# Kernel tuning notes

Hardware: AMD Instinct MI355X
Metric: run time of the kernel (lower is better)

## Reference

```python
import jax, jax.numpy as jnp
import numpy as np

NUM_HEADS = 16
HEAD_DIM = 80  # embed_dim 1280 / 16


def setup_inputs() -> dict:
    key = jax.random.key(0)
    ks = jax.random.split(key, 5)
    E = NUM_HEADS * HEAD_DIM
    sq, b = 1024, 8
    x = jax.random.normal(ks[0], (sq, b, E), dtype=jnp.float32)
    w_in = jax.random.normal(ks[1], (E, 3 * E), dtype=jnp.float32) * (E ** -0.5)
    b_in = jax.random.normal(ks[2], (3 * E,), dtype=jnp.float32) * 0.01
    w_out = jax.random.normal(ks[3], (E, E), dtype=jnp.float32) * (E ** -0.5)
    b_out = jax.random.normal(ks[4], (E,), dtype=jnp.float32) * 0.01
    return {"x": x, "w_in": w_in, "b_in": b_in, "w_out": w_out, "b_out": b_out}


def reference(x, w_in, b_in, w_out, b_out):
    sq, b, E = x.shape
    H, D = NUM_HEADS, HEAD_DIM
    norm_factor = jnp.asarray(D ** 0.5, x.dtype)
    # in_proj: [sq, b, 3E] -> [sq, b, H, 3D], split into q/k/v along last dim
    mixed = (x @ w_in + b_in).reshape(sq, b, H, 3 * D)
    q, k, v = jnp.split(mixed, 3, axis=-1)  # each [sq, b, H, D]
    # merge (b, H) and move to batch-of-bmm layout [b*H, sq, D]
    q = q.reshape(sq, b * H, D).transpose(1, 0, 2) / norm_factor
    k = k.reshape(sq, b * H, D).transpose(1, 0, 2)
    v = v.reshape(sq, b * H, D).transpose(1, 0, 2)
    scores = jnp.einsum('nqd,nkd->nqk', q, k)  # [b*H, sq, sq]
    probs = jax.nn.softmax(scores, axis=-1)
    ctx = jnp.einsum('nqk,nkd->nqd', probs, v)  # [b*H, sq, D]
    # [b, H, sq, D] -> [sq, b, H, D] -> [sq, b, E]
    ctx = ctx.reshape(b, H, sq, D).transpose(2, 0, 1, 3).reshape(sq, b, E)
    return ctx @ w_out + b_out
```

## Files before the change

### kernel.cpp

```cpp
#include <hip/hip_runtime.h>

#define DEVI __device__ __forceinline__

typedef _Float16 f16x8 __attribute__((ext_vector_type(8)));
typedef _Float16 f16x4v __attribute__((ext_vector_type(4)));
typedef _Float16 f16x2 __attribute__((ext_vector_type(2)));
typedef float f32x4 __attribute__((ext_vector_type(4)));

DEVI void gl16(const void* g, void* l) {
  __builtin_amdgcn_global_load_lds((const __attribute__((address_space(1))) void*)g,
                                   (__attribute__((address_space(3))) void*)l, 16, 0, 0);
}

#define VMCNT(N) asm volatile("s_waitcnt vmcnt(" #N ")" ::: "memory")
#define LGKM0() asm volatile("s_waitcnt lgkmcnt(0)" ::: "memory")
#define BARRIER() asm volatile("s_barrier" ::: "memory")

__global__ __launch_bounds__(256) void k_cvt(const float* __restrict__ in, _Float16* __restrict__ out, int n4) {
  int i = blockIdx.x * 256 + threadIdx.x;
  int stride = gridDim.x * 256;
  for (; i < n4; i += stride) {
    float4 v = ((const float4*)in)[i];
    f16x4v h = { (_Float16)v.x, (_Float16)v.y, (_Float16)v.z, (_Float16)v.w };
    ((f16x4v*)out)[i] = h;
  }
}

__global__ __launch_bounds__(256) void k_transpose(const float* __restrict__ in, _Float16* __restrict__ out,
                                                   int R, int C) {
  __shared__ float t[32][33];
  int cb = blockIdx.x * 32, rb = blockIdx.y * 32;
  int tx = threadIdx.x & 31, ty = threadIdx.x >> 5;
  #pragma unroll
  for (int i = ty; i < 32; i += 8) t[i][tx] = in[(size_t)(rb + i) * C + cb + tx];
  __syncthreads();
  #pragma unroll
  for (int i = ty; i < 32; i += 8) out[(size_t)(cb + i) * R + rb + tx] = (_Float16)t[tx][i];
}


#define MM(NLO, AF, BF) do {                                                                       \
    __builtin_amdgcn_s_setprio(1);                                                                 \
    _Pragma("unroll")                                                                              \
    for (int m_ = 0; m_ < 8; m_++) {                                                               \
      acc[m_][NLO]     = __builtin_amdgcn_mfma_f32_16x16x32_f16(AF[m_], BF[NLO],     acc[m_][NLO],     0, 0, 0); \
      acc[m_][NLO + 1] = __builtin_amdgcn_mfma_f32_16x16x32_f16(AF[m_], BF[NLO + 1], acc[m_][NLO + 1], 0, 0, 0); \
    }                                                                                              \
    __builtin_amdgcn_s_setprio(0);                                                                 \
  } while (0)

#define LDA(KT, KK, DST) do {                                                                      \
    const _Float16* bas_ = &smem[(size_t)((((KT) & 1) * 2) + wr) * 8192];                          \
    _Pragma("unroll")                                                                              \
    for (int m_ = 0; m_ < 8; m_++)                                                                 \
      DST[m_] = *(const f16x8*)&bas_[(m_ * 16 + ln) * 64 + (((((KK) * 4) + g) ^ chB) << 3)];       \
  } while (0)

#define LDB(KT, KK, DST) do {                                                                      \
    const _Float16* bas_ = &smem[32768 + (size_t)((((KT) & 1) * 2) + (wc >> 1)) * 8192];           \
    _Pragma("unroll")                                                                              \
    for (int n_ = 0; n_ < 4; n_++)                                                                 \
      DST[n_] = *(const f16x8*)&bas_[((wc & 1) * 64 + n_ * 16 + ln) * 64 + (((((KK) * 4) + g) ^ chB) << 3)]; \
  } while (0)

template<int M, int N, int K>
__global__ __launch_bounds__(512, 2) void k_gemm8(const _Float16* __restrict__ A, const _Float16* __restrict__ BT,
                                                  const float* __restrict__ bias,
                                                  _Float16* __restrict__ qo, _Float16* __restrict__ ko,
                                                  _Float16* __restrict__ vo) {
  extern __shared__ _Float16 smem[];
  constexpr int NT = K / 64;
  constexpr int NI = NT / 2;
  const int tid = threadIdx.x;
  const int w = tid >> 6, lane = tid & 63, ln = lane & 15, g = lane >> 4;
  const int wr = w >> 2, wc = w & 3;
  const int l8 = lane >> 3, l7 = lane & 7;
  const int stChunk = (l7 ^ l8) << 3;
  const int chB = ln & 7;

  constexpr int MT = M / 256;
  const int xcd = blockIdx.x & 7;
  const int i = blockIdx.x >> 3;
  const int bm0 = (xcd * (MT / 8) + (i & 3)) * 256;
  const int bn0 = (i >> 2) * 256;

  auto stgA = [&](int kt, int hh) {
    _Float16* ldsb = &smem[(size_t)((kt & 1) * 2 + hh) * 8192 + w * 1024];
    const _Float16* g0 = &A[(size_t)(bm0 + hh * 128 + w * 16 + l8) * K + kt * 64 + stChunk];
    gl16(g0, ldsb);
    gl16(g0 + (size_t)8 * K, ldsb + 512);
  };
  auto stgB = [&](int kt, int hh) {
    _Float16* ldsb = &smem[32768 + (size_t)((kt & 1) * 2 + hh) * 8192 + w * 1024];
    const _Float16* g0 = &BT[(size_t)(bn0 + hh * 128 + w * 16 + l8) * K + kt * 64 + stChunk];
    gl16(g0, ldsb);
    gl16(g0 + (size_t)8 * K, ldsb + 512);
  };

  f32x4 acc[8][4] = {};
  f16x8 a0[8], a1[8], b0[4], b1[4];

  stgB(0, 0); stgB(0, 1); stgA(0, 0); stgA(0, 1);
  stgB(1, 0); stgB(1, 1); stgA(1, 0);
  VMCNT(6);
  BARRIER();
  LDA(0, 0, a0); LDB(0, 0, b0);

  for (int it = 0; it < NI; ++it) {
    const int T0 = 2 * it, T1 = 2 * it + 1;
    const int S0 = (T0 + 2 < NT) ? T0 + 2 : 0;
    const int S1 = (T1 + 2 < NT) ? T1 + 2 : 1;
    LDB(T0, 1, b1);
    stgA(T1, 1);
    BARRIER();
    MM(0, a0, b0);
    LGKM0(); BARRIER();
    LDA(T0, 1, a1);
    stgB(S0, 0);
    BARRIER();
    MM(2, a0, b0);
    LGKM0(); BARRIER();
    stgB(S0, 1);
    BARRIER();
    MM(0, a1, b1);
    VMCNT(4);
    LGKM0(); BARRIER();
    LDA(T1, 0, a0); LDB(T1, 0, b0);
    stgA(S0, 0);
    BARRIER();
    MM(2, a1, b1);
    LGKM0(); BARRIER();
    LDB(T1, 1, b1);
    stgA(S0, 1);
    BARRIER();
    MM(0, a0, b0);
    LGKM0(); BARRIER();
    LDA(T1, 1, a1);
    stgB(S1, 0);
    BARRIER();
    MM(2, a0, b0);
    LGKM0(); BARRIER();
    stgB(S1, 1);
    BARRIER();
    MM(0, a1, b1);
    VMCNT(4);
    LGKM0(); BARRIER();
    LDA(S0, 0, a0); LDB(S0, 0, b0);
    stgA(S1, 0);
    BARRIER();
    MM(2, a1, b1);
    LGKM0(); BARRIER();
  }

  VMCNT(0);
  BARRIER();
  _Float16* sH = smem;
  #pragma unroll
  for (int n = 0; n < 4; n++) {
    int col = wc * 64 + n * 16 + ln;
    int gcol = bn0 + col;
    float bv = bias[gcol];
    int hq = gcol / 240;
    int tt = gcol - hq * 240;
    float scl = (tt < 80) ? 0.11180339887498948f : 1.0f;
    #pragma unroll
    for (int m = 0; m < 8; m++) {
      #pragma unroll
      for (int r = 0; r < 4; r++) {
        int row = wr * 128 + m * 16 + 4 * g + r;
        sH[row * 256 + col] = (_Float16)((acc[m][n][r] + bv) * scl);
      }
    }
  }
  LGKM0();
  BARRIER();
  #pragma unroll
  for (int i2 = 0; i2 < 16; i2++) {
    int id = tid + 512 * i2;
    int row = id >> 5, c8 = id & 31;
    f16x8 v = *(const f16x8*)&sH[row * 256 + c8 * 8];
    int gcol = bn0 + c8 * 8;
    int grow = bm0 + row;
    int hq = gcol / 240;
    int tt = gcol - hq * 240;
    int reg = tt / 80;
    int cc = tt - reg * 80;
    int s = grow >> 3;
    int head = (grow & 7) * 16 + hq;
    _Float16* dst = (reg == 0) ? qo : (reg == 1) ? ko : vo;
    *(f16x8*)&dst[(size_t)(head * 1024 + s) * 80 + cc] = v;
  }
}

template<int M, int N, int K>
__global__ __launch_bounds__(256) void k_gemm(const _Float16* __restrict__ A, const _Float16* __restrict__ BT,
                                              const float* __restrict__ bias, float* __restrict__ outF) {
  __shared__ _Float16 Al[128 * 32];
  __shared__ _Float16 Bl[128 * 32];
  const int tid = threadIdx.x;
  const int w = tid >> 6, lane = tid & 63, ln = lane & 15, g = lane >> 4;
  const int bm0 = blockIdx.x * 128, bn0 = blockIdx.y * 128;
  const int wm = (w >> 1) * 64, wn = (w & 1) * 64;
  const int r0 = tid >> 2, c0 = (tid & 3) * 8;
  f32x4 acc[4][4] = {};
  for (int kt = 0; kt < K; kt += 32) {
    __syncthreads();
    gl16(&A[(size_t)(bm0 + r0) * K + kt + c0],      &Al[(w * 64) * 8]);
    gl16(&A[(size_t)(bm0 + r0 + 64) * K + kt + c0], &Al[(256 + w * 64) * 8]);
    gl16(&BT[(size_t)(bn0 + r0) * K + kt + c0],      &Bl[(w * 64) * 8]);
    gl16(&BT[(size_t)(bn0 + r0 + 64) * K + kt + c0], &Bl[(256 + w * 64) * 8]);
    __syncthreads();
    f16x8 af[4], bf[4];
    #pragma unroll
    for (int i = 0; i < 4; i++) af[i] = *(const f16x8*)&Al[(wm + i * 16 + ln) * 32 + g * 8];
    #pragma unroll
    for (int i = 0; i < 4; i++) bf[i] = *(const f16x8*)&Bl[(wn + i * 16 + ln) * 32 + g * 8];
    #pragma unroll
    for (int i = 0; i < 4; i++)
      #pragma unroll
      for (int j = 0; j < 4; j++)
        acc[i][j] = __builtin_amdgcn_mfma_f32_16x16x32_f16(af[i], bf[j], acc[i][j], 0, 0, 0);
  }
  #pragma unroll
  for (int j = 0; j < 4; j++) {
    int col = bn0 + wn + j * 16 + ln;
    float bv = bias[col];
    #pragma unroll
    for (int i = 0; i < 4; i++) {
      int mb = bm0 + wm + i * 16 + 4 * g;
      #pragma unroll
      for (int r = 0; r < 4; r++)
        outF[(size_t)(mb + r) * N + col] = acc[i][j][r] + bv;
    }
  }
}

__global__ __launch_bounds__(256) void k_vtrans(const _Float16* __restrict__ vb, _Float16* __restrict__ vT) {
  __shared__ _Float16 t[64][81];
  int head = blockIdx.x >> 4;
  int sb = (blockIdx.x & 15) * 64;
  for (int idx = threadIdx.x; idx < 64 * 80; idx += 256) {
    int s = idx / 80, d = idx - s * 80;
    t[s][d] = vb[(head * 1024 + sb + s) * 80 + d];
  }
  __syncthreads();
  for (int idx = threadIdx.x; idx < 80 * 64; idx += 256) {
    int d = idx >> 6, s = idx & 63;
    vT[(head * 80 + d) * 1024 + sb + s] = t[s][d];
  }
}

__global__ __launch_bounds__(512) void k_attn(const _Float16* __restrict__ qb, const _Float16* __restrict__ kb,
                                              const _Float16* __restrict__ vT, _Float16* __restrict__ ctxg) {
  __shared__ _Float16 Kl[64 * 104];
  __shared__ _Float16 Vl[80 * 72];
  __shared__ _Float16 Pl[128 * 72];
  const int tid = threadIdx.x;
  const int w = tid >> 6, lane = tid & 63, ln = lane & 15, g = lane >> 4;
  const int xcd = blockIdx.x & 7;
  const int j = blockIdx.x >> 3;
  const int head = xcd + 8 * (j & 15);
  const int s0 = (j >> 4) * 128;
  const int bb = head >> 4, h = head & 15;

  const int qrow = s0 + w * 16 + ln;
  f16x8 qf[3];
  qf[0] = *(const f16x8*)&qb[(size_t)(head * 1024 + qrow) * 80 + g * 8];
  qf[1] = *(const f16x8*)&qb[(size_t)(head * 1024 + qrow) * 80 + 32 + g * 8];
  {
    f16x8 z = {};
    qf[2] = (g < 2) ? *(const f16x8*)&qb[(size_t)(head * 1024 + qrow) * 80 + 64 + g * 8] : z;
  }

  f32x4 ctxa[5] = {};
  float m_run = -INFINITY, l_run = 0.f;

  for (int kt2 = 0; kt2 < 16; ++kt2) {
    __syncthreads();
    for (int c = tid; c < 832; c += 512) {
      int row = c / 13, ch = c - row * 13;
      uint4 z4 = {0, 0, 0, 0};
      uint4 v4 = (ch < 10) ? *(const uint4*)&kb[(size_t)(head * 1024 + kt2 * 64 + row) * 80 + ch * 8] : z4;
      *(uint4*)&Kl[row * 104 + ch * 8] = v4;
    }
    for (int c = tid; c < 640; c += 512) {
      int row = c >> 3, ch = c & 7;
      *(uint4*)&Vl[row * 72 + ch * 8] = *(const uint4*)&vT[(size_t)(head * 80 + row) * 1024 + kt2 * 64 + ch * 8];
    }
    __syncthreads();
    f32x4 sc[4] = {};
    #pragma unroll
    for (int t16 = 0; t16 < 4; ++t16)
      #pragma unroll
      for (int dc = 0; dc < 3; ++dc) {
        f16x8 kf = *(const f16x8*)&Kl[(t16 * 16 + ln) * 104 + dc * 32 + g * 8];
        sc[t16] = __builtin_amdgcn_mfma_f32_16x16x32_f16(kf, qf[dc], sc[t16], 0, 0, 0);
      }
    float tm = -INFINITY;
    #pragma unroll
    for (int t16 = 0; t16 < 4; ++t16)
      #pragma unroll
      for (int r = 0; r < 4; ++r) tm = fmaxf(tm, sc[t16][r]);
    tm = fmaxf(tm, __shfl_xor(tm, 16));
    tm = fmaxf(tm, __shfl_xor(tm, 32));
    float mnew = fmaxf(m_run, tm);
    float fac = __expf(m_run - mnew);
    float ps = 0.f;
    #pragma unroll
    for (int t16 = 0; t16 < 4; ++t16) {
      float p0 = __expf(sc[t16][0] - mnew);
      float p1 = __expf(sc[t16][1] - mnew);
      float p2 = __expf(sc[t16][2] - mnew);
      float p3 = __expf(sc[t16][3] - mnew);
      ps += (p0 + p1) + (p2 + p3);
      int off = (w * 16 + ln) * 72 + t16 * 16 + g * 4;
      f16x2 w01 = { (_Float16)p0, (_Float16)p1 };
      f16x2 w23 = { (_Float16)p2, (_Float16)p3 };
      *(f16x2*)&Pl[off] = w01;
      *(f16x2*)&Pl[off + 2] = w23;
    }
    ps += __shfl_xor(ps, 16);
    ps += __shfl_xor(ps, 32);
    l_run = l_run * fac + ps;
    m_run = mnew;
    #pragma unroll
    for (int r = 0; r < 4; ++r) {
      float fr = __shfl(fac, 4 * g + r);
      #pragma unroll
      for (int nt = 0; nt < 5; ++nt) ctxa[nt][r] *= fr;
    }
    #pragma unroll
    for (int kb4 = 0; kb4 < 2; ++kb4) {
      f16x8 pf = *(const f16x8*)&Pl[(w * 16 + ln) * 72 + kb4 * 32 + g * 8];
      #pragma unroll
      for (int nt = 0; nt < 5; ++nt) {
        f16x8 vf = *(const f16x8*)&Vl[(nt * 16 + ln) * 72 + kb4 * 32 + g * 8];
        ctxa[nt] = __builtin_amdgcn_mfma_f32_16x16x32_f16(pf, vf, ctxa[nt], 0, 0, 0);
      }
    }
  }
  #pragma unroll
  for (int r = 0; r < 4; ++r) {
    float lr = __shfl(l_run, 4 * g + r);
    float inv = 1.f / lr;
    int s = s0 + w * 16 + 4 * g + r;
    int base = (s * 8 + bb) * 1280 + h * 80;
    #pragma unroll
    for (int nt = 0; nt < 5; ++nt)
      ctxg[base + nt * 16 + ln] = (_Float16)(ctxa[nt][r] * inv);
  }
}

extern "C" void kernel_launch(void* const* d_in, const int* in_sizes, int n_in,
                              void* d_out, int out_size, void* d_ws, size_t ws_size,
                              hipStream_t stream) {
  const float* x     = (const float*)d_in[0];
  const float* w_in  = (const float*)d_in[1];
  const float* b_in  = (const float*)d_in[2];
  const float* w_out = (const float*)d_in[3];
  const float* b_out = (const float*)d_in[4];
  float* out = (float*)d_out;

  char* ws = (char*)d_ws;
  size_t off = 0;
  auto carve = [&](size_t bytes) -> void* {
    void* p = ws + off;
    off += (bytes + 255) & ~(size_t)255;
    return p;
  };
  _Float16* xb     = (_Float16*)carve(8192ull * 1280 * 2);
  _Float16* w_inT  = (_Float16*)carve(3840ull * 1280 * 2);
  _Float16* w_outT = (_Float16*)carve(1280ull * 1280 * 2);
  _Float16* qb     = (_Float16*)carve(128ull * 1024 * 80 * 2);
  _Float16* kbuf   = (_Float16*)carve(128ull * 1024 * 80 * 2);
  _Float16* vb     = (_Float16*)carve(128ull * 1024 * 80 * 2);
  _Float16* vT     = (_Float16*)carve(128ull * 1024 * 80 * 2);
  _Float16* ctxg   = (_Float16*)carve(8192ull * 1280 * 2);
  if (off > ws_size) return;

  hipFuncSetAttribute(reinterpret_cast<const void*>(&k_gemm8<8192, 3840, 1280>),
                      hipFuncAttributeMaxDynamicSharedMemorySize, 131072);

  k_cvt<<<2048, 256, 0, stream>>>(x, xb, 8192 * 1280 / 4);
  k_transpose<<<dim3(120, 40), 256, 0, stream>>>(w_in, w_inT, 1280, 3840);
  k_transpose<<<dim3(40, 40), 256, 0, stream>>>(w_out, w_outT, 1280, 1280);

  k_gemm8<8192, 3840, 1280><<<480, 512, 131072, stream>>>(xb, w_inT, b_in, qb, kbuf, vb);
  k_vtrans<<<2048, 256, 0, stream>>>(vb, vT);
  k_attn<<<1024, 512, 0, stream>>>(qb, kbuf, vT, ctxg);
  k_gemm<8192, 1280, 1280><<<dim3(64, 10), 256, 0, stream>>>(ctxg, w_outT, b_out, out);
}
```

Baseline: 270.2 us.

## Restructure attention kernel with 32x32 MFMA, larger query tile and prefetched K/V

The attention kernel now processes 256 query rows per block (32 per wave) and computes QK^T with 32x32x16 MFMAs, so each K tile loaded into LDS is reused by more queries. K/V tiles for the next step are prefetched into registers and staged into LDS (V double-buffered) while the current tile is consumed, replacing the old load-sync-compute loop. The log2(e) factor is folded into the Q scale in the projection epilogue so softmax can use exp2, and P is packed to fp16 with cvt_pkrtz. In exchange the kernel uses more registers and about 79KB of dynamic LDS, and launches half as many blocks, which lowers occupancy.

```diff
diff --git a/kernel.cpp b/kernel.cpp
--- a/kernel.cpp
+++ b/kernel.cpp
@@ -5,7 +5,9 @@
 typedef _Float16 f16x8 __attribute__((ext_vector_type(8)));
 typedef _Float16 f16x4v __attribute__((ext_vector_type(4)));
 typedef _Float16 f16x2 __attribute__((ext_vector_type(2)));
+typedef __fp16 fp16x2 __attribute__((ext_vector_type(2)));
 typedef float f32x4 __attribute__((ext_vector_type(4)));
+typedef float f32x16 __attribute__((ext_vector_type(16)));
 
 DEVI void gl16(const void* g, void* l) {
   __builtin_amdgcn_global_load_lds((const __attribute__((address_space(1))) void*)g,
@@ -15,6 +17,11 @@
 #define VMCNT(N) asm volatile("s_waitcnt vmcnt(" #N ")" ::: "memory")
 #define LGKM0() asm volatile("s_waitcnt lgkmcnt(0)" ::: "memory")
 #define BARRIER() asm volatile("s_barrier" ::: "memory")
+
+DEVI unsigned pk2(float a, float b) {
+  fp16x2 t = __builtin_amdgcn_cvt_pkrtz(a, b);
+  return __builtin_bit_cast(unsigned, t);
+}
 
 __global__ __launch_bounds__(256) void k_cvt(const float* __restrict__ in, _Float16* __restrict__ out, int n4) {
   int i = blockIdx.x * 256 + threadIdx.x;
@@ -162,7 +169,7 @@
     float bv = bias[gcol];
     int hq = gcol / 240;
     int tt = gcol - hq * 240;
-    float scl = (tt < 80) ? 0.11180339887498948f : 1.0f;
+    float scl = (tt < 80) ? (0.11180339887498948f * 1.4426950408889634f) : 1.0f;
     #pragma unroll
     for (int m = 0; m < 8; m++) {
       #pragma unroll
@@ -250,105 +257,147 @@
   }
 }
 
-__global__ __launch_bounds__(512) void k_attn(const _Float16* __restrict__ qb, const _Float16* __restrict__ kb,
-                                              const _Float16* __restrict__ vT, _Float16* __restrict__ ctxg) {
-  __shared__ _Float16 Kl[64 * 104];
-  __shared__ _Float16 Vl[80 * 72];
-  __shared__ _Float16 Pl[128 * 72];
+__global__ __launch_bounds__(512, 4) void k_attn(const _Float16* __restrict__ qb, const _Float16* __restrict__ kb,
+                                                 const _Float16* __restrict__ vT, _Float16* __restrict__ ctxg) {
+  extern __shared__ _Float16 smem[];
+  _Float16* Kb  = smem;
+  _Float16* Vb0 = smem + 5632;
+  _Float16* Vb1 = smem + 5632 + 5760;
+  _Float16* Pb  = smem + 5632 + 11520;
+
   const int tid = threadIdx.x;
-  const int w = tid >> 6, lane = tid & 63, ln = lane & 15, g = lane >> 4;
+  const int w = tid >> 6, lane = tid & 63;
+  const int ln = lane & 15, g = (lane >> 4) & 3;
+  const int l32 = lane & 31, h = lane >> 5;
   const int xcd = blockIdx.x & 7;
   const int j = blockIdx.x >> 3;
   const int head = xcd + 8 * (j & 15);
-  const int s0 = (j >> 4) * 128;
-  const int bb = head >> 4, h = head & 15;
-
-  const int qrow = s0 + w * 16 + ln;
-  f16x8 qf[3];
-  qf[0] = *(const f16x8*)&qb[(size_t)(head * 1024 + qrow) * 80 + g * 8];
-  qf[1] = *(const f16x8*)&qb[(size_t)(head * 1024 + qrow) * 80 + 32 + g * 8];
-  {
-    f16x8 z = {};
-    qf[2] = (g < 2) ? *(const f16x8*)&qb[(size_t)(head * 1024 + qrow) * 80 + 64 + g * 8] : z;
-  }
-
-  f32x4 ctxa[5] = {};
+  const int s0 = (j >> 4) * 256;
+  const int bb = head >> 4, h16 = head & 15;
+
+  const int kc1 = (tid < 128) ? tid + 512 : tid;
+  const int kr0 = tid / 10, kh0 = tid - kr0 * 10;
+  const int kr1 = kc1 / 10, kh1 = kc1 - kr1 * 10;
+  const int vr0 = tid >> 3, vh0 = tid & 7;
+  const int vr1 = kc1 >> 3, vh1 = kc1 & 7;
+  const size_t kbase = (size_t)head * 1024 * 80;
+  const size_t vbase = (size_t)head * 80 * 1024;
+
+  uint4 krA, krB, vrA, vrB;
+  auto issue = [&](int kt) {
+    const _Float16* kg = kb + kbase + (size_t)(kt * 64) * 80;
+    krA = *(const uint4*)(kg + kr0 * 80 + kh0 * 8);
+    krB = *(const uint4*)(kg + kr1 * 80 + kh1 * 8);
+    const _Float16* vg = vT + vbase + kt * 64;
+    vrA = *(const uint4*)(vg + (size_t)vr0 * 1024 + vh0 * 8);
+    vrB = *(const uint4*)(vg + (size_t)vr1 * 1024 + vh1 * 8);
+  };
+  auto stage = [&](int kt) {
+    *(uint4*)(Kb + kr0 * 88 + kh0 * 8) = krA;
+    *(uint4*)(Kb + kr1 * 88 + kh1 * 8) = krB;
+    _Float16* vd = (kt & 1) ? Vb1 : Vb0;
+    *(uint4*)(vd + vr0 * 72 + vh0 * 8) = vrA;
+    *(uint4*)(vd + vr1 * 72 + vh1 * 8) = vrB;
+  };
+
+  const int qrow = s0 + w * 32 + l32;
+  f16x8 qf[5];
+  #pragma unroll
+  for (int s = 0; s < 5; s++)
+    qf[s] = *(const f16x8*)&qb[(size_t)(head * 1024 + qrow) * 80 + s * 16 + h * 8];
+
+  f32x4 ctxa[2][5] = {};
   float m_run = -INFINITY, l_run = 0.f;
 
-  for (int kt2 = 0; kt2 < 16; ++kt2) {
-    __syncthreads();
-    for (int c = tid; c < 832; c += 512) {
-      int row = c / 13, ch = c - row * 13;
-      uint4 z4 = {0, 0, 0, 0};
-      uint4 v4 = (ch < 10) ? *(const uint4*)&kb[(size_t)(head * 1024 + kt2 * 64 + row) * 80 + ch * 8] : z4;
-      *(uint4*)&Kl[row * 104 + ch * 8] = v4;
-    }
-    for (int c = tid; c < 640; c += 512) {
-      int row = c >> 3, ch = c & 7;
-      *(uint4*)&Vl[row * 72 + ch * 8] = *(const uint4*)&vT[(size_t)(head * 80 + row) * 1024 + kt2 * 64 + ch * 8];
-    }
-    __syncthreads();
-    f32x4 sc[4] = {};
-    #pragma unroll
-    for (int t16 = 0; t16 < 4; ++t16)
-      #pragma unroll
-      for (int dc = 0; dc < 3; ++dc) {
-        f16x8 kf = *(const f16x8*)&Kl[(t16 * 16 + ln) * 104 + dc * 32 + g * 8];
-        sc[t16] = __builtin_amdgcn_mfma_f32_16x16x32_f16(kf, qf[dc], sc[t16], 0, 0, 0);
+  issue(0);
+  stage(0);
+  LGKM0();
+  BARRIER();
+  issue(1);
+
+  for (int kt = 0; kt < 16; ++kt) {
+    f32x16 sc[2] = {};
+    __builtin_amdgcn_s_setprio(1);
+    #pragma unroll
+    for (int t = 0; t < 2; ++t)
+      #pragma unroll
+      for (int s = 0; s < 5; ++s) {
+        f16x8 kf = *(const f16x8*)&Kb[(t * 32 + l32) * 88 + s * 16 + h * 8];
+        sc[t] = __builtin_amdgcn_mfma_f32_32x32x16_f16(kf, qf[s], sc[t], 0, 0, 0);
       }
+    __builtin_amdgcn_s_setprio(0);
+    BARRIER();
+
     float tm = -INFINITY;
     #pragma unroll
-    for (int t16 = 0; t16 < 4; ++t16)
-      #pragma unroll
-      for (int r = 0; r < 4; ++r) tm = fmaxf(tm, sc[t16][r]);
-    tm = fmaxf(tm, __shfl_xor(tm, 16));
+    for (int t = 0; t < 2; ++t)
+      #pragma unroll
+      for (int r = 0; r < 16; ++r) tm = fmaxf(tm, sc[t][r]);
     tm = fmaxf(tm, __shfl_xor(tm, 32));
     float mnew = fmaxf(m_run, tm);
-    float fac = __expf(m_run - mnew);
+    float fac = exp2f(m_run - mnew);
     float ps = 0.f;
-    #pragma unroll
-    for (int t16 = 0; t16 < 4; ++t16) {
-      float p0 = __expf(sc[t16][0] - mnew);
-      float p1 = __expf(sc[t16][1] - mnew);
-      float p2 = __expf(sc[t16][2] - mnew);
-      float p3 = __expf(sc[t16][3] - mnew);
-      ps += (p0 + p1) + (p2 + p3);
-      int off = (w * 16 + ln) * 72 + t16 * 16 + g * 4;
-      f16x2 w01 = { (_Float16)p0, (_Float16)p1 };
-      f16x2 w23 = { (_Float16)p2, (_Float16)p3 };
-      *(f16x2*)&Pl[off] = w01;
-      *(f16x2*)&Pl[off + 2] = w23;
-    }
-    ps += __shfl_xor(ps, 16);
+    const int prow = (w * 32 + l32) * 88;
+    #pragma unroll
+    for (int t = 0; t < 2; ++t)
+      #pragma unroll
+      for (int rq = 0; rq < 4; ++rq) {
+        float p0 = exp2f(sc[t][rq * 4 + 0] - mnew);
+        float p1 = exp2f(sc[t][rq * 4 + 1] - mnew);
+        float p2 = exp2f(sc[t][rq * 4 + 2] - mnew);
+        float p3 = exp2f(sc[t][rq * 4 + 3] - mnew);
+        ps += (p0 + p1) + (p2 + p3);
+        unsigned long long u = (unsigned long long)pk2(p0, p1) | ((unsigned long long)pk2(p2, p3) << 32);
+        *(unsigned long long*)&Pb[prow + t * 32 + rq * 8 + h * 4] = u;
+      }
     ps += __shfl_xor(ps, 32);
     l_run = l_run * fac + ps;
     m_run = mnew;
     #pragma unroll
+    for (int rb = 0; rb < 2; ++rb)
+      #pragma unroll
+      for (int r = 0; r < 4; ++r) {
+        float fr = __shfl(fac, rb * 16 + 4 * g + r);
+        #pragma unroll
+        for (int nt = 0; nt < 5; ++nt) ctxa[rb][nt][r] *= fr;
+      }
+    LGKM0();
+
+    {
+      const _Float16* vcur = (kt & 1) ? Vb1 : Vb0;
+      __builtin_amdgcn_s_setprio(1);
+      #pragma unroll
+      for (int kb4 = 0; kb4 < 2; ++kb4) {
+        f16x8 pf0 = *(const f16x8*)&Pb[(w * 32 + ln) * 88 + kb4 * 32 + g * 8];
+        f16x8 pf1 = *(const f16x8*)&Pb[(w * 32 + 16 + ln) * 88 + kb4 * 32 + g * 8];
+        #pragma unroll
+        for (int nt = 0; nt < 5; ++nt) {
+          f16x8 vf = *(const f16x8*)&vcur[(nt * 16 + ln) * 72 + kb4 * 32 + g * 8];
+          ctxa[0][nt] = __builtin_amdgcn_mfma_f32_16x16x32_f16(pf0, vf, ctxa[0][nt], 0, 0, 0);
+          ctxa[1][nt] = __builtin_amdgcn_mfma_f32_16x16x32_f16(pf1, vf, ctxa[1][nt], 0, 0, 0);
+        }
+      }
+      __builtin_amdgcn_s_setprio(0);
+    }
+
+    stage(kt + 1);
+    LGKM0();
+    BARRIER();
+    issue(kt + 2 < 16 ? kt + 2 : 15);
+  }
+
+  #pragma unroll
+  for (int rb = 0; rb < 2; ++rb)
+    #pragma unroll
     for (int r = 0; r < 4; ++r) {
-      float fr = __shfl(fac, 4 * g + r);
-      #pragma unroll
-      for (int nt = 0; nt < 5; ++nt) ctxa[nt][r] *= fr;
+      float lr = __shfl(l_run, rb * 16 + 4 * g + r);
+      float inv = 1.f / lr;
+      int s = s0 + w * 32 + rb * 16 + 4 * g + r;
+      int base = (s * 8 + bb) * 1280 + h16 * 80;
+      #pragma unroll
+      for (int nt = 0; nt < 5; ++nt)
+        ctxg[base + nt * 16 + ln] = (_Float16)(ctxa[rb][nt][r] * inv);
     }
-    #pragma unroll
-    for (int kb4 = 0; kb4 < 2; ++kb4) {
-      f16x8 pf = *(const f16x8*)&Pl[(w * 16 + ln) * 72 + kb4 * 32 + g * 8];
-      #pragma unroll
-      for (int nt = 0; nt < 5; ++nt) {
-        f16x8 vf = *(const f16x8*)&Vl[(nt * 16 + ln) * 72 + kb4 * 32 + g * 8];
-        ctxa[nt] = __builtin_amdgcn_mfma_f32_16x16x32_f16(pf, vf, ctxa[nt], 0, 0, 0);
-      }
-    }
-  }
-  #pragma unroll
-  for (int r = 0; r < 4; ++r) {
-    float lr = __shfl(l_run, 4 * g + r);
-    float inv = 1.f / lr;
-    int s = s0 + w * 16 + 4 * g + r;
-    int base = (s * 8 + bb) * 1280 + h * 80;
-    #pragma unroll
-    for (int nt = 0; nt < 5; ++nt)
-      ctxg[base + nt * 16 + ln] = (_Float16)(ctxa[nt][r] * inv);
-  }
 }
 
 extern "C" void kernel_launch(void* const* d_in, const int* in_sizes, int n_in,
@@ -380,6 +429,8 @@
 
   hipFuncSetAttribute(reinterpret_cast<const void*>(&k_gemm8<8192, 3840, 1280>),
                       hipFuncAttributeMaxDynamicSharedMemorySize, 131072);
+  hipFuncSetAttribute(reinterpret_cast<const void*>(&k_attn),
+                      hipFuncAttributeMaxDynamicSharedMemorySize, 79360);
 
   k_cvt<<<2048, 256, 0, stream>>>(x, xb, 8192 * 1280 / 4);
   k_transpose<<<dim3(120, 40), 256, 0, stream>>>(w_in, w_inT, 1280, 3840);
@@ -387,6 +438,6 @@
 
   k_gemm8<8192, 3840, 1280><<<480, 512, 131072, stream>>>(xb, w_inT, b_in, qb, kbuf, vb);
   k_vtrans<<<2048, 256, 0, stream>>>(vb, vT);
-  k_attn<<<1024, 512, 0, stream>>>(qb, kbuf, vT, ctxg);
+  k_attn<<<512, 512, 79360, stream>>>(qb, kbuf, vT, ctxg);
   k_gemm<8192, 1280, 1280><<<dim3(64, 10), 256, 0, stream>>>(ctxg, w_outT, b_out, out);
 }
```

Result: no change. 266.9 us (-1.2%).
